# Kernel optimization log

Measured on AMD Instinct MI355X. Metric: run time of the kernel, lower is better.

Reference implementation:

```python
import jax, jax.numpy as jnp
import numpy as np

B, T, E, H = 256, 256, 384, 64

def setup_inputs() -> dict:
    key = jax.random.key(0)
    ks = jax.random.split(key, 4)
    s = 1.0 / np.sqrt(E)
    return {
        "x":  jax.random.normal(ks[0], (B, T, E), dtype=jnp.float32),
        "Wq": jax.random.normal(ks[1], (E, H), dtype=jnp.float32) * s,
        "bq": jnp.zeros((H,), dtype=jnp.float32),
        "Wk": jax.random.normal(ks[2], (E, H), dtype=jnp.float32) * s,
        "bk": jnp.zeros((H,), dtype=jnp.float32),
        "Wv": jax.random.normal(ks[3], (E, H), dtype=jnp.float32) * s,
        "bv": jnp.zeros((H,), dtype=jnp.float32),
    }

def reference(x, Wq, bq, Wk, bk, Wv, bv):
    # QKV projections: [B,T,E] @ [E,H] -> [B,T,H]
    q = x @ Wq + bq
    k = x @ Wk + bk
    v = x @ Wv + bv
    # attention scores (NOTE: original has no 1/sqrt(d) scaling)
    wei = jnp.einsum('bth,bsh->bts', q, k)  # [B,T,T]
    causal = jnp.tril(jnp.ones((T, T), dtype=bool))
    wei = jnp.where(causal, wei, -jnp.inf)
    wei = jax.nn.softmax(wei, axis=-1)
    # dropout is identity in eval mode
    out = jnp.einsum('bts,bsh->bth', wei, v)  # [B,T,H]
    return out
```

## Files before the change

kernel.cpp:

```cpp
#include <hip/hip_runtime.h>
#include <math.h>

#define Bb 256
#define Tt 256
#define Ee 384
#define Hh 64

typedef __attribute__((ext_vector_type(8))) short bf16x8;
typedef __attribute__((ext_vector_type(4))) float f32x4;

__device__ inline short f2bf(float f) {
    unsigned u = __float_as_uint(f);
    u += 0x7FFFu + ((u >> 16) & 1);
    return (short)(u >> 16);
}
__device__ inline float bf2f(short s) {
    return __uint_as_float(((unsigned)(unsigned short)s) << 16);
}

#define MFMA16(a, b, c) __builtin_amdgcn_mfma_f32_16x16x32_bf16((a), (b), (c), 0, 0, 0)

#define A_HI 0
#define A_LO 16384
#define B_HI 32768
#define B_LO 45056
#define K_HI 0
#define K_LO 32768
#define VF   65536
#define QH   98304
#define QL   116736
#define PBASE 98304
#define SMEM_BYTES 135168

__global__ __launch_bounds__(1024) void head_fused(
    const float* __restrict__ x,
    const float* __restrict__ Wq, const float* __restrict__ bq,
    const float* __restrict__ Wk, const float* __restrict__ bk,
    const float* __restrict__ Wv, const float* __restrict__ bv,
    float* __restrict__ out)
{
    __shared__ __align__(16) unsigned char smem[SMEM_BYTES];

    const int b    = blockIdx.x;
    const int tid  = threadIdx.x;
    const int w    = tid >> 6;
    const int lane = tid & 63;
    const int quad = lane >> 4;
    const int nl   = lane & 15;
    const int wi   = w >> 1;
    const int wj   = w & 1;

    f32x4 acc0[6], acc1[6];
    #pragma unroll
    for (int i = 0; i < 6; ++i) { acc0[i] = (f32x4){0,0,0,0}; acc1[i] = (f32x4){0,0,0,0}; }

    const float4* x4 = reinterpret_cast<const float4*>(x + (size_t)b * Tt * Ee);

    for (int ec = 0; ec < 12; ++ec) {
        __syncthreads();
        {
            int mg = tid >> 2, koct = tid & 3;
            float4 f0 = x4[mg * 96 + ec * 8 + koct * 2];
            float4 f1 = x4[mg * 96 + ec * 8 + koct * 2 + 1];
            float v[8] = {f0.x, f0.y, f0.z, f0.w, f1.x, f1.y, f1.z, f1.w};
            bf16x8 hi8, lo8;
            #pragma unroll
            for (int j = 0; j < 8; ++j) {
                short h = f2bf(v[j]);
                hi8[j] = h;
                lo8[j] = f2bf(v[j] - bf2f(h));
            }
            int off = (mg >> 4) * 1024 + (koct * 16 + (mg & 15)) * 16;
            *reinterpret_cast<bf16x8*>(smem + A_HI + off) = hi8;
            *reinterpret_cast<bf16x8*>(smem + A_LO + off) = lo8;
        }
        #pragma unroll
        for (int rep = 0; rep < 2; ++rep) {
            int idx = tid + rep * 1024;
            if (idx < 1536) {
                int e = idx / 48, hq = idx - e * 48;
                int h = hq * 4;
                const float* Wm = (h < 64) ? Wq : (h < 128 ? Wk : Wv);
                int hh = h & 63;
                float4 f = *reinterpret_cast<const float4*>(Wm + (ec * 32 + e) * 64 + hh);
                int tile = h >> 4, n0 = h & 15, j = e & 7, sb = (e >> 3) * 16 + n0;
                float vv[4] = {f.x, f.y, f.z, f.w};
                #pragma unroll
                for (int c = 0; c < 4; ++c) {
                    short hi = f2bf(vv[c]);
                    short lo = f2bf(vv[c] - bf2f(hi));
                    int a = tile * 1024 + (sb + c) * 16 + j * 2;
                    *reinterpret_cast<short*>(smem + B_HI + a) = hi;
                    *reinterpret_cast<short*>(smem + B_LO + a) = lo;
                }
            }
        }
        __syncthreads();
        int ao = (2 * wi) * 1024 + lane * 16;
        bf16x8 a0h = *reinterpret_cast<bf16x8*>(smem + A_HI + ao);
        bf16x8 a0l = *reinterpret_cast<bf16x8*>(smem + A_LO + ao);
        bf16x8 a1h = *reinterpret_cast<bf16x8*>(smem + A_HI + ao + 1024);
        bf16x8 a1l = *reinterpret_cast<bf16x8*>(smem + A_LO + ao + 1024);
        #pragma unroll
        for (int ct = 0; ct < 6; ++ct) {
            int tb = (wj * 6 + ct) * 1024 + lane * 16;
            bf16x8 bh = *reinterpret_cast<bf16x8*>(smem + B_HI + tb);
            bf16x8 bl = *reinterpret_cast<bf16x8*>(smem + B_LO + tb);
            acc0[ct] = MFMA16(a0h, bh, acc0[ct]);
            acc0[ct] = MFMA16(a0l, bh, acc0[ct]);
            acc0[ct] = MFMA16(a0h, bl, acc0[ct]);
            acc1[ct] = MFMA16(a1h, bh, acc1[ct]);
            acc1[ct] = MFMA16(a1l, bh, acc1[ct]);
            acc1[ct] = MFMA16(a1h, bl, acc1[ct]);
        }
    }
    __syncthreads();

    #pragma unroll
    for (int ct = 0; ct < 6; ++ct) {
        int col = (wj * 6 + ct) * 16 + nl;
        float bias = (col < 64) ? bq[col] : (col < 128 ? bk[col - 64] : bv[col - 128]);
        #pragma unroll
        for (int r = 0; r < 4; ++r) { acc0[ct][r] += bias; acc1[ct][r] += bias; }
    }

    #pragma unroll
    for (int ct = 0; ct < 6; ++ct) {
        int col = (wj * 6 + ct) * 16 + nl;
        #pragma unroll
        for (int rt = 0; rt < 2; ++rt) {
            #pragma unroll
            for (int r = 0; r < 4; ++r) {
                float val = (rt ? acc1[ct] : acc0[ct])[r];
                int s = wi * 32 + rt * 16 + quad * 4 + r;
                if (col >= 64 && col < 128) {
                    int h = col - 64;
                    int addr = ((s >> 4) * 2 + (h >> 5)) * 1024
                             + ((((h & 31) >> 3) * 16 + (s & 15)) * 8 + (h & 7)) * 2;
                    short hi = f2bf(val);
                    short lo = f2bf(val - bf2f(hi));
                    *reinterpret_cast<short*>(smem + K_HI + addr) = hi;
                    *reinterpret_cast<short*>(smem + K_LO + addr) = lo;
                } else if (col >= 128) {
                    int h = col - 128, sl = s & 31;
                    int addr = ((s >> 5) * 4 + (h >> 4)) * 1024
                             + (((sl >> 3) * 16 + (h & 15)) * 8 + (sl & 7)) * 2;
                    *reinterpret_cast<short*>(smem + VF + addr) = f2bf(val);
                }
            }
        }
    }

    auto writeQ = [&]() {
        #pragma unroll
        for (int ct = 0; ct < 4; ++ct) {
            #pragma unroll
            for (int rt = 0; rt < 2; ++rt) {
                #pragma unroll
                for (int r = 0; r < 4; ++r) {
                    float val = (rt ? acc1[ct] : acc0[ct])[r];
                    int s = wi * 32 + rt * 16 + quad * 4 + r;
                    int rloc = s & 127;
                    int h = ct * 16 + nl;
                    short hi = f2bf(val);
                    short lo = f2bf(val - bf2f(hi));
                    *reinterpret_cast<short*>(smem + QH + (rloc * 72 + h) * 2) = hi;
                    *reinterpret_cast<short*>(smem + QL + (rloc * 72 + h) * 2) = lo;
                }
            }
        }
    };
    bf16x8 qh0, qh1, ql0, ql1;
    auto readQ = [&]() {
        int rloc = (16 * w + nl) & 127;
        int base = rloc * 144;
        qh0 = *reinterpret_cast<bf16x8*>(smem + QH + base + quad * 16);
        qh1 = *reinterpret_cast<bf16x8*>(smem + QH + base + 64 + quad * 16);
        ql0 = *reinterpret_cast<bf16x8*>(smem + QL + base + quad * 16);
        ql1 = *reinterpret_cast<bf16x8*>(smem + QL + base + 64 + quad * 16);
    };

    if (wj == 0 && wi < 4) writeQ();
    __syncthreads();
    if (w < 8) readQ();
    __syncthreads();
    if (wj == 0 && wi >= 4) writeQ();
    __syncthreads();
    if (w >= 8) readQ();
    __syncthreads();

    f32x4 oacc[4];
    #pragma unroll
    for (int i = 0; i < 4; ++i) oacc[i] = (f32x4){0,0,0,0};
    float lsum = 0.f;
    const int t0 = w * 16;
    unsigned char* pb = smem + PBASE + w * 1344;
    const int npairs = (w >> 1) + 1;

    for (int p = 0; p < npairs; ++p) {
        #pragma unroll
        for (int hf = 0; hf < 2; ++hf) {
            int st = 2 * p + hf;
            f32x4 sacc = (f32x4){0,0,0,0};
            int kb = st * 2048 + lane * 16;
            bf16x8 kh0 = *reinterpret_cast<bf16x8*>(smem + K_HI + kb);
            bf16x8 kh1 = *reinterpret_cast<bf16x8*>(smem + K_HI + kb + 1024);
            bf16x8 kl0 = *reinterpret_cast<bf16x8*>(smem + K_LO + kb);
            bf16x8 kl1 = *reinterpret_cast<bf16x8*>(smem + K_LO + kb + 1024);
            sacc = MFMA16(qh0, kh0, sacc);
            sacc = MFMA16(qh1, kh1, sacc);
            sacc = MFMA16(ql0, kh0, sacc);
            sacc = MFMA16(ql1, kh1, sacc);
            sacc = MFMA16(qh0, kl0, sacc);
            sacc = MFMA16(qh1, kl1, sacc);
            int sg = st * 16 + nl;
            #pragma unroll
            for (int r = 0; r < 4; ++r) {
                int tg = t0 + quad * 4 + r;
                float pv = (sg <= tg) ? __expf(sacc[r]) : 0.f;
                *reinterpret_cast<short*>(pb + ((quad * 4 + r) * 40 + hf * 16 + nl) * 2) = f2bf(pv);
            }
        }
        asm volatile("s_waitcnt lgkmcnt(0)" ::: "memory");
        bf16x8 pa = *reinterpret_cast<bf16x8*>(pb + (nl * 40 + quad * 8) * 2);
        float ls = 0.f;
        #pragma unroll
        for (int j = 0; j < 8; ++j) ls += bf2f(pa[j]);
        ls += __shfl_xor(ls, 16);
        ls += __shfl_xor(ls, 32);
        lsum += ls;
        int vb = p * 4096 + lane * 16;
        #pragma unroll
        for (int nt = 0; nt < 4; ++nt) {
            bf16x8 vf = *reinterpret_cast<bf16x8*>(smem + VF + vb + nt * 1024);
            oacc[nt] = MFMA16(pa, vf, oacc[nt]);
        }
    }

    float* lb_ = reinterpret_cast<float*>(pb + 1280);
    if (lane < 16) lb_[lane] = lsum;
    asm volatile("s_waitcnt lgkmcnt(0)" ::: "memory");
    float* ob = out + (size_t)b * Tt * Hh + (size_t)t0 * Hh;
    #pragma unroll
    for (int r = 0; r < 4; ++r) {
        float inv = 1.0f / lb_[quad * 4 + r];
        #pragma unroll
        for (int nt = 0; nt < 4; ++nt)
            ob[(quad * 4 + r) * 64 + nt * 16 + nl] = oacc[nt][r] * inv;
    }
}

extern "C" void kernel_launch(void* const* d_in, const int* in_sizes, int n_in,
                              void* d_out, int out_size, void* d_ws, size_t ws_size,
                              hipStream_t stream) {
    const float* x  = (const float*)d_in[0];
    const float* Wq = (const float*)d_in[1];
    const float* bq = (const float*)d_in[2];
    const float* Wk = (const float*)d_in[3];
    const float* bk = (const float*)d_in[4];
    const float* Wv = (const float*)d_in[5];
    const float* bv = (const float*)d_in[6];
    float* out = (float*)d_out;
    hipLaunchKernelGGL(head_fused, dim3(Bb), dim3(1024), 0, stream,
                       x, Wq, bq, Wk, bk, Wv, bv, out);
}
```

Measured before the change: 205.5 us.

## Prefetch next x/W chunk into registers and split score MFMA chains

Loads of the next E-chunk of x and the weights into registers are issued right after the barrier, so global latency overlaps the MFMA work on the current chunk. The per-thread load mapping is remapped so each thread writes one contiguous 16-byte bf16x8 to shared memory instead of scattered 2-byte stores. The QK^T score accumulation is split into two independent accumulator chains to shorten MFMA dependency latency. Costs are extra registers for the prefetch buffers and a strided scalar weight load pattern.

```diff
diff --git a/kernel.cpp b/kernel.cpp
--- a/kernel.cpp
+++ b/kernel.cpp
@@ -56,13 +56,26 @@
 
     const float4* x4 = reinterpret_cast<const float4*>(x + (size_t)b * Tt * Ee);
 
+    const int At  = ((tid >> 6) << 4) + (tid & 15);
+    const int Ako = (tid >> 4) & 3;
+    const float4* xsrc = x4 + At * 96 + Ako * 2;
+    const int wtile = tid >> 6, weo = (tid >> 4) & 3, wn0 = tid & 15;
+    const int wcol  = wtile * 16 + wn0;
+    const float* Wsel = (wcol < 64) ? Wq : ((wcol < 128) ? Wk : Wv);
+    const float* wsrc = Wsel + (wcol & 63) + weo * 8 * 64;
+
+    float4 pa0 = xsrc[0], pa1 = xsrc[1];
+    float pw[8];
+    if (tid < 768) {
+        #pragma unroll
+        for (int j = 0; j < 8; ++j) pw[j] = wsrc[j * 64];
+    }
+
     for (int ec = 0; ec < 12; ++ec) {
         __syncthreads();
+
         {
-            int mg = tid >> 2, koct = tid & 3;
-            float4 f0 = x4[mg * 96 + ec * 8 + koct * 2];
-            float4 f1 = x4[mg * 96 + ec * 8 + koct * 2 + 1];
-            float v[8] = {f0.x, f0.y, f0.z, f0.w, f1.x, f1.y, f1.z, f1.w};
+            float v[8] = {pa0.x, pa0.y, pa0.z, pa0.w, pa1.x, pa1.y, pa1.z, pa1.w};
             bf16x8 hi8, lo8;
             #pragma unroll
             for (int j = 0; j < 8; ++j) {
@@ -70,32 +83,31 @@
                 hi8[j] = h;
                 lo8[j] = f2bf(v[j] - bf2f(h));
             }
-            int off = (mg >> 4) * 1024 + (koct * 16 + (mg & 15)) * 16;
-            *reinterpret_cast<bf16x8*>(smem + A_HI + off) = hi8;
-            *reinterpret_cast<bf16x8*>(smem + A_LO + off) = lo8;
-        }
-        #pragma unroll
-        for (int rep = 0; rep < 2; ++rep) {
-            int idx = tid + rep * 1024;
-            if (idx < 1536) {
-                int e = idx / 48, hq = idx - e * 48;
-                int h = hq * 4;
-                const float* Wm = (h < 64) ? Wq : (h < 128 ? Wk : Wv);
-                int hh = h & 63;
-                float4 f = *reinterpret_cast<const float4*>(Wm + (ec * 32 + e) * 64 + hh);
-                int tile = h >> 4, n0 = h & 15, j = e & 7, sb = (e >> 3) * 16 + n0;
-                float vv[4] = {f.x, f.y, f.z, f.w};
+            *reinterpret_cast<bf16x8*>(smem + A_HI + tid * 16) = hi8;
+            *reinterpret_cast<bf16x8*>(smem + A_LO + tid * 16) = lo8;
+        }
+        if (tid < 768) {
+            bf16x8 hi8, lo8;
+            #pragma unroll
+            for (int j = 0; j < 8; ++j) {
+                short h = f2bf(pw[j]);
+                hi8[j] = h;
+                lo8[j] = f2bf(pw[j] - bf2f(h));
+            }
+            *reinterpret_cast<bf16x8*>(smem + B_HI + tid * 16) = hi8;
+            *reinterpret_cast<bf16x8*>(smem + B_LO + tid * 16) = lo8;
+        }
+        __syncthreads();
+
+        if (ec < 11) {
+            pa0 = xsrc[(ec + 1) * 8];
+            pa1 = xsrc[(ec + 1) * 8 + 1];
+            if (tid < 768) {
                 #pragma unroll
-                for (int c = 0; c < 4; ++c) {
-                    short hi = f2bf(vv[c]);
-                    short lo = f2bf(vv[c] - bf2f(hi));
-                    int a = tile * 1024 + (sb + c) * 16 + j * 2;
-                    *reinterpret_cast<short*>(smem + B_HI + a) = hi;
-                    *reinterpret_cast<short*>(smem + B_LO + a) = lo;
-                }
-            }
-        }
-        __syncthreads();
+                for (int j = 0; j < 8; ++j) pw[j] = wsrc[(ec + 1) * 2048 + j * 64];
+            }
+        }
+
         int ao = (2 * wi) * 1024 + lane * 16;
         bf16x8 a0h = *reinterpret_cast<bf16x8*>(smem + A_HI + ao);
         bf16x8 a0l = *reinterpret_cast<bf16x8*>(smem + A_LO + ao);
@@ -201,23 +213,24 @@
         #pragma unroll
         for (int hf = 0; hf < 2; ++hf) {
             int st = 2 * p + hf;
-            f32x4 sacc = (f32x4){0,0,0,0};
+            f32x4 s0 = (f32x4){0,0,0,0}, s1 = (f32x4){0,0,0,0};
             int kb = st * 2048 + lane * 16;
             bf16x8 kh0 = *reinterpret_cast<bf16x8*>(smem + K_HI + kb);
             bf16x8 kh1 = *reinterpret_cast<bf16x8*>(smem + K_HI + kb + 1024);
             bf16x8 kl0 = *reinterpret_cast<bf16x8*>(smem + K_LO + kb);
             bf16x8 kl1 = *reinterpret_cast<bf16x8*>(smem + K_LO + kb + 1024);
-            sacc = MFMA16(qh0, kh0, sacc);
-            sacc = MFMA16(qh1, kh1, sacc);
-            sacc = MFMA16(ql0, kh0, sacc);
-            sacc = MFMA16(ql1, kh1, sacc);
-            sacc = MFMA16(qh0, kl0, sacc);
-            sacc = MFMA16(qh1, kl1, sacc);
+            s0 = MFMA16(qh0, kh0, s0);
+            s1 = MFMA16(qh1, kh1, s1);
+            s0 = MFMA16(ql0, kh0, s0);
+            s1 = MFMA16(ql1, kh1, s1);
+            s0 = MFMA16(qh0, kl0, s0);
+            s1 = MFMA16(qh1, kl1, s1);
             int sg = st * 16 + nl;
             #pragma unroll
             for (int r = 0; r < 4; ++r) {
                 int tg = t0 + quad * 4 + r;
-                float pv = (sg <= tg) ? __expf(sacc[r]) : 0.f;
+                float sv = s0[r] + s1[r];
+                float pv = (sg <= tg) ? __expf(sv) : 0.f;
                 *reinterpret_cast<short*>(pb + ((quad * 4 + r) * 40 + hf * 16 + nl) * 2) = f2bf(pv);
             }
         }
```

Result: faster. 185.0 us (-10.0%).
